# Optimization experiments

Measured on AMD Instinct MI355X. Metric: run time of the kernel, lower is better.

Reference implementation:

```python
import jax, jax.numpy as jnp
import numpy as np

N_HEADS = 16
N_KV_HEADS = 4
HEAD_DIM = 128  # d_model // n_heads = 2048 // 16
ROPE_THETA = 10000.0


def _rope_cos_sin(T, D, dtype):
    inv_freq = 1.0 / (ROPE_THETA ** (jnp.arange(0, D, 2, dtype=jnp.float32) / D))
    t = jnp.arange(T, dtype=jnp.float32)
    freqs = jnp.outer(t, inv_freq)               # [T, D/2]
    emb = jnp.concatenate([freqs, freqs], axis=-1)  # [T, D]
    return jnp.cos(emb).astype(dtype), jnp.sin(emb).astype(dtype)


def _rotate_half(x):
    x1, x2 = jnp.split(x, 2, axis=-1)
    return jnp.concatenate([-x2, x1], axis=-1)


def setup_inputs() -> dict:
    key = jax.random.key(0)
    k1, k2, k3, k4, k5 = jax.random.split(key, 5)
    B, T, C = 2, 2048, 2048
    H, KV, D = N_HEADS, N_KV_HEADS, HEAD_DIM
    s = 0.02
    return {
        "x": jax.random.normal(k1, (B, T, C), dtype=jnp.float32),
        "Wq": jax.random.normal(k2, (C, H * D), dtype=jnp.float32) * s,
        "Wk": jax.random.normal(k3, (C, KV * D), dtype=jnp.float32) * s,
        "Wv": jax.random.normal(k4, (C, KV * D), dtype=jnp.float32) * s,
        "Wo": jax.random.normal(k5, (H * D, C), dtype=jnp.float32) * s,
    }


def reference(x, Wq, Wk, Wv, Wo):
    B, T, C = x.shape
    H, KV, D = N_HEADS, N_KV_HEADS, HEAD_DIM
    G = H // KV
    scale = D ** -0.5

    q = (x @ Wq).reshape(B, T, H, D).transpose(0, 2, 1, 3)    # [B,H,T,D]
    k = (x @ Wk).reshape(B, T, KV, D).transpose(0, 2, 1, 3)   # [B,KV,T,D]
    v = (x @ Wv).reshape(B, T, KV, D).transpose(0, 2, 1, 3)   # [B,KV,T,D]

    cos, sin = _rope_cos_sin(T, D, x.dtype)  # [T,D] each, broadcasts over B,H
    q = q * cos + _rotate_half(q) * sin
    k = k * cos + _rotate_half(k) * sin

    # repeat_interleave kv heads to match query heads
    k = jnp.repeat(k, G, axis=1)  # [B,H,T,D]
    v = jnp.repeat(v, G, axis=1)  # [B,H,T,D]

    scores = jnp.einsum('bhqd,bhkd->bhqk', q, k) * scale  # [B,H,T,T]
    causal = jnp.tril(jnp.ones((T, T), dtype=bool))
    scores = jnp.where(causal, scores, jnp.finfo(scores.dtype).min)
    attn = jax.nn.softmax(scores, axis=-1)

    out = jnp.einsum('bhqk,bhkd->bhqd', attn, v)           # [B,H,T,D]
    out = out.transpose(0, 2, 1, 3).reshape(B, T, H * D)    # [B,T,C]
    return out @ Wo
```

## Files before the change

### kernel.cpp

```cpp
#include <hip/hip_runtime.h>
#include <cstdint>
#include <cstddef>

typedef __attribute__((ext_vector_type(4))) float f32x4;
typedef __attribute__((ext_vector_type(8))) short s16x8;
typedef __attribute__((ext_vector_type(4))) short s16x4;

#define B_  2
#define T_  2048
#define C_  2048
#define H_  16
#define KV_ 4
#define D_  128
#define M_  4096

static __device__ __forceinline__ float bf2f(ushort u){
  union { float f; uint32_t u; } x; x.u = ((uint32_t)u) << 16; return x.f;
}
static __device__ __forceinline__ ushort f2bf(float f){
  union { float f; uint32_t u; } x; x.f = f;
  uint32_t r = x.u + 0x7FFF + ((x.u >> 16) & 1);
  return (ushort)(r >> 16);
}

static __device__ __forceinline__ void gl_lds16(const ushort* g, ushort* s){
  __builtin_amdgcn_global_load_lds((const __attribute__((address_space(1))) void*)g,
                                   (__attribute__((address_space(3))) void*)s, 16, 0, 0);
}

__global__ void cvt_f32_bf16(const float* __restrict__ in, ushort* __restrict__ out, int n4){
  int idx = blockIdx.x * blockDim.x + threadIdx.x;
  int stride = gridDim.x * blockDim.x;
  for (int i = idx; i < n4; i += stride){
    float4 v = ((const float4*)in)[i];
    s16x4 o;
    o[0] = (short)f2bf(v.x); o[1] = (short)f2bf(v.y);
    o[2] = (short)f2bf(v.z); o[3] = (short)f2bf(v.w);
    ((s16x4*)out)[i] = o;
  }
}

__global__ void transpose_all(const float* __restrict__ Wq, const float* __restrict__ Wk,
                              const float* __restrict__ Wv, const float* __restrict__ Wo,
                              ushort* __restrict__ Wcat, ushort* __restrict__ Wot){
  __shared__ float tile[32][33];
  int bx = blockIdx.x;
  const float* W; ushort* Wt; int N; int n0;
  if (bx < 64)      { W = Wq; Wt = Wcat;                          N = 2048; n0 = bx * 32; }
  else if (bx < 80) { W = Wk; Wt = Wcat + (size_t)2048 * 2048;    N = 512;  n0 = (bx - 64) * 32; }
  else if (bx < 96) { W = Wv; Wt = Wcat + (size_t)2560 * 2048;    N = 512;  n0 = (bx - 80) * 32; }
  else              { W = Wo; Wt = Wot;                           N = 2048; n0 = (bx - 96) * 32; }
  int k0 = blockIdx.y * 32;
  int tx = threadIdx.x, ty = threadIdx.y;
  #pragma unroll
  for (int r = 0; r < 4; r++)
    tile[ty + 8*r][tx] = W[(size_t)(k0 + ty + 8*r) * N + n0 + tx];
  __syncthreads();
  #pragma unroll
  for (int r = 0; r < 4; r++)
    Wt[(size_t)(n0 + ty + 8*r) * 2048 + k0 + tx] = f2bf(tile[tx][ty + 8*r]);
}

template<int MODE>
__global__ __launch_bounds__(512)
void gemm_deep(const ushort* __restrict__ A, const ushort* __restrict__ Bt,
               void* __restrict__ C0, void* __restrict__ C1, void* __restrict__ C2,
               int N, int Kd, int nbx){
  __shared__ __align__(16) ushort Abuf[4][8192];
  __shared__ __align__(16) ushort Bbuf[4][8192];
  int tid = threadIdx.x, w = tid >> 6, l = tid & 63;
  int l15 = l & 15, l4 = l >> 4;

  int cpx = gridDim.x >> 3;
  int logical = (blockIdx.x & 7) * cpx + (blockIdx.x >> 3);
  int bx = logical % nbx, by = logical / nbx;
  int rblk = by * 128, cblk = bx * 128;
  int wm = w & 1, wn = w >> 1;

  int sr = tid >> 3;
  int sc = ((tid & 7) * 8) ^ ((sr & 7) << 3);
  const ushort* gA = A  + (size_t)(rblk + sr) * Kd + sc;
  const ushort* gB = Bt + (size_t)(cblk + sr) * Kd + sc;
  size_t rowK = (size_t)64 * Kd;
  int wb = w * 512;

  auto stage = [&](int t){
    int bsel = t & 3; int koff = t * 64;
    gl_lds16(gA + koff,        &Abuf[bsel][wb]);
    gl_lds16(gA + rowK + koff, &Abuf[bsel][4096 + wb]);
    gl_lds16(gB + koff,        &Bbuf[bsel][wb]);
    gl_lds16(gB + rowK + koff, &Bbuf[bsel][4096 + wb]);
  };

  int arow = wm * 64 + l15;
  int brow = wn * 32 + l15;
  int kx0 = (l4 * 8) ^ ((l15 & 7) << 3);
  int kx1 = (32 + l4 * 8) ^ ((l15 & 7) << 3);

  f32x4 acc[4][2] = {};

  auto phase = [&](int t, int dostage, int vm){
    const ushort* Ab = Abuf[t & 3];
    const ushort* Bb = Bbuf[t & 3];
    s16x8 a[4][2], b[2][2];
    #pragma unroll
    for (int m = 0; m < 4; m++){
      a[m][0] = *(const s16x8*)(Ab + (arow + m*16) * 64 + kx0);
      a[m][1] = *(const s16x8*)(Ab + (arow + m*16) * 64 + kx1);
    }
    #pragma unroll
    for (int n = 0; n < 2; n++){
      b[n][0] = *(const s16x8*)(Bb + (brow + n*16) * 64 + kx0);
      b[n][1] = *(const s16x8*)(Bb + (brow + n*16) * 64 + kx1);
    }
    if (dostage) stage(t + 3);
    if (vm == 8)      { asm volatile("s_waitcnt vmcnt(8)" ::: "memory"); }
    else if (vm == 4) { asm volatile("s_waitcnt vmcnt(4)" ::: "memory"); }
    else if (vm == 0) { asm volatile("s_waitcnt vmcnt(0)" ::: "memory"); }
    asm volatile("s_waitcnt lgkmcnt(0)" ::: "memory");
    __builtin_amdgcn_sched_barrier(0);
    __builtin_amdgcn_s_barrier();
    __builtin_amdgcn_s_setprio(1);
    #pragma unroll
    for (int m = 0; m < 4; m++)
      #pragma unroll
      for (int n = 0; n < 2; n++){
        acc[m][n] = __builtin_amdgcn_mfma_f32_16x16x32_bf16(a[m][0], b[n][0], acc[m][n], 0, 0, 0);
        acc[m][n] = __builtin_amdgcn_mfma_f32_16x16x32_bf16(a[m][1], b[n][1], acc[m][n], 0, 0, 0);
      }
    __builtin_amdgcn_s_setprio(0);
  };

  stage(0); stage(1); stage(2);
  asm volatile("s_waitcnt vmcnt(8)" ::: "memory");
  __builtin_amdgcn_s_barrier();

  int nt = Kd >> 6;
  #pragma unroll 1
  for (int t = 0; t < nt - 3; ++t) phase(t, 1, 8);
  phase(nt - 3, 0, 4);
  phase(nt - 2, 0, 0);
  phase(nt - 1, 0, -1);

  #pragma unroll
  for (int m = 0; m < 4; m++){
    #pragma unroll
    for (int n = 0; n < 2; n++){
      #pragma unroll
      for (int j = 0; j < 4; j++){
        int row = rblk + wm*64 + m*16 + l4*4 + j;
        int col = cblk + wn*32 + n*16 + l15;
        float v = acc[m][n][j];
        if (MODE == 0){
          ((float*)C0)[(size_t)row * N + col] = v;
        } else {
          int t = row & (T_ - 1), bb = row >> 11;
          ushort bv = f2bf(v);
          if (col < 2048){
            int hh = col >> 7, d = col & 127;
            ((ushort*)C0)[(((size_t)(bb * H_ + hh)) * T_ + t) * D_ + d] = bv;
          } else if (col < 2560){
            int c2 = col - 2048;
            int hh = c2 >> 7, d = c2 & 127;
            ((ushort*)C1)[(((size_t)(bb * KV_ + hh)) * T_ + t) * D_ + d] = bv;
          } else {
            int c2 = col - 2560;
            int hh = c2 >> 7, d = c2 & 127;
            ((ushort*)C2)[(((size_t)(bb * KV_ + hh)) * D_ + d) * T_ + t] = bv;
          }
        }
      }
    }
  }
}

__global__ __launch_bounds__(256)
void rope_all(ushort* __restrict__ Qb, ushort* __restrict__ Kb, float sq){
  int y = blockIdx.y;
  ushort* X; int bh; float scale;
  if (y < B_ * H_){ X = Qb; bh = y;           scale = sq;  }
  else            { X = Kb; bh = y - B_ * H_; scale = 1.f; }
  int tr = threadIdx.x >> 4;
  int j  = threadIdx.x & 15;
  int t  = blockIdx.x * 16 + tr;
  ushort* row = X + ((size_t)bh * T_ + t) * D_;
  s16x4 lo = *(const s16x4*)(row + j*4);
  s16x4 hi = *(const s16x4*)(row + 64 + j*4);
  s16x4 olo, ohi;
  #pragma unroll
  for (int i = 0; i < 4; i++){
    int d = j*4 + i;
    float invf = exp2f(-(float)d * 0.2076205059304602f);
    float s, c;
    __sincosf((float)t * invf, &s, &c);
    float q1 = bf2f((ushort)lo[i]);
    float q2 = bf2f((ushort)hi[i]);
    olo[i] = (short)f2bf((q1 * c - q2 * s) * scale);
    ohi[i] = (short)f2bf((q2 * c + q1 * s) * scale);
  }
  *(s16x4*)(row + j*4) = olo;
  *(s16x4*)(row + 64 + j*4) = ohi;
}

__global__ __launch_bounds__(512, 4)
void attn_kernel4(const ushort* __restrict__ Q, const ushort* __restrict__ Kc,
                  const ushort* __restrict__ Vt, ushort* __restrict__ O){
  __shared__ __align__(16) ushort Ks[64 * 128];
  __shared__ __align__(16) ushort Vs[128 * 64];
  __shared__ __align__(16) ushort Ps[8 * 16 * 64];
  int bid = blockIdx.x;
  int i  = bid >> 3;
  int qt = (i < 32) ? (63 - i) : (i - 32);
  int sub = bid & 7;
  int b = sub >> 2, kvh = sub & 3;
  int tid = threadIdx.x, w = tid >> 6, l = tid & 63;
  int l15 = l & 15, l4 = l >> 4;
  int sw3 = (l15 & 7) << 3;
  int q0 = qt * 32;
  int hq = kvh * 4 + (w >> 1);
  int qrow0 = q0 + (w & 1) * 16;
  int qrow = qrow0 + l15;

  s16x8 qf[4];
  const ushort* qbase = Q + (((size_t)(b * H_ + hq)) * T_ + qrow) * D_;
  #pragma unroll
  for (int kk = 0; kk < 4; kk++)
    qf[kk] = *(const s16x8*)(qbase + kk * 32 + l4 * 8);

  f32x4 oacc[8] = {};
  float mrun = -1e30f;
  float rsum = 0.f;
  const float THR = 11.5415603f;
  ushort* Pw = Ps + w * (16 * 64) + l15 * 64;

  const ushort* kbase = Kc + ((size_t)(b * KV_ + kvh)) * T_ * D_;
  const ushort* vbase = Vt + ((size_t)(b * KV_ + kvh)) * D_ * T_;
  int jmax = (q0 + 31) >> 6;

  int kr0 = tid >> 4, kcb = tid & 15;
  int vd0 = tid >> 3, vtb = tid & 7;
  int ksoff = kr0 * 128 + ((kcb * 8) ^ ((kr0 & 7) << 3));
  int vsoff = vd0 * 64  + ((vtb * 8) ^ ((vd0 & 7) << 3));
  const ushort* kg = kbase + (size_t)kr0 * D_ + kcb * 8;
  const ushort* vg = vbase + (size_t)vd0 * T_ + vtb * 8;

  s16x8 kreg0, kreg1, vreg0, vreg1;
  kreg0 = *(const s16x8*)(kg);
  kreg1 = *(const s16x8*)(kg + (size_t)32 * D_);
  vreg0 = *(const s16x8*)(vg);
  vreg1 = *(const s16x8*)(vg + (size_t)64 * T_);

  for (int jt = 0; jt <= jmax; jt++){
    __syncthreads();
    *(s16x8*)(Ks + ksoff)            = kreg0;
    *(s16x8*)(Ks + ksoff + 32 * 128) = kreg1;
    *(s16x8*)(Vs + vsoff)            = vreg0;
    *(s16x8*)(Vs + vsoff + 64 * 64)  = vreg1;
    __syncthreads();
    if (jt < jmax){
      int k1 = (jt + 1) * 64;
      kreg0 = *(const s16x8*)(kg + (size_t)k1 * D_);
      kreg1 = *(const s16x8*)(kg + (size_t)(k1 + 32) * D_);
      vreg0 = *(const s16x8*)(vg + k1);
      vreg1 = *(const s16x8*)(vg + (size_t)64 * T_ + k1);
    }
    int k0 = jt * 64;

    f32x4 sacc[4] = {};
    __builtin_amdgcn_s_setprio(1);
    #pragma unroll
    for (int kk = 0; kk < 4; kk++){
      #pragma unroll
      for (int n = 0; n < 4; n++){
        s16x8 kf = *(const s16x8*)(Ks + (16*n + l15) * 128 + ((kk*32 + l4*8) ^ sw3));
        sacc[n] = __builtin_amdgcn_mfma_f32_16x16x32_bf16(kf, qf[kk], sacc[n], 0, 0, 0);
      }
    }
    __builtin_amdgcn_s_setprio(0);
    if (jt == jmax){
      #pragma unroll
      for (int n = 0; n < 4; n++)
        #pragma unroll
        for (int j = 0; j < 4; j++){
          int kcol = k0 + 16*n + 4*l4 + j;
          if (kcol > qrow) sacc[n][j] = -1e30f;
        }
    }
    float mloc = -1e30f;
    #pragma unroll
    for (int n = 0; n < 4; n++)
      #pragma unroll
      for (int j = 0; j < 4; j++)
        mloc = fmaxf(mloc, sacc[n][j]);
    if (__any((int)(mloc > mrun + THR))){
      float m2 = fmaxf(mloc, __shfl_xor(mloc, 16));
      m2 = fmaxf(m2, __shfl_xor(m2, 32));
      float mnew = fmaxf(mrun, m2);
      float alpha = exp2f(mrun - mnew);
      mrun = mnew;
      rsum *= alpha;
      #pragma unroll
      for (int n8 = 0; n8 < 8; n8++)
        #pragma unroll
        for (int j = 0; j < 4; j++)
          oacc[n8][j] *= alpha;
    }
    #pragma unroll
    for (int n = 0; n < 4; n++){
      s16x4 pk;
      #pragma unroll
      for (int j = 0; j < 4; j++){
        float p = exp2f(sacc[n][j] - mrun);
        rsum += p;
        pk[j] = (short)f2bf(p);
      }
      *(s16x4*)(Pw + ((16*n + 4*l4) ^ sw3)) = pk;
    }
    __builtin_amdgcn_s_setprio(1);
    #pragma unroll
    for (int kk = 0; kk < 2; kk++){
      s16x8 pf = *(const s16x8*)(Pw + ((kk*32 + l4*8) ^ sw3));
      #pragma unroll
      for (int n8 = 0; n8 < 8; n8++){
        s16x8 vf = *(const s16x8*)(Vs + (16*n8 + l15) * 64 + ((kk*32 + l4*8) ^ sw3));
        oacc[n8] = __builtin_amdgcn_mfma_f32_16x16x32_bf16(vf, pf, oacc[n8], 0, 0, 0);
      }
    }
    __builtin_amdgcn_s_setprio(0);
  }

  rsum += __shfl_xor(rsum, 16);
  rsum += __shfl_xor(rsum, 32);
  float inv = 1.f / rsum;
  ushort* obase = O + ((size_t)(b * T_ + qrow)) * C_ + hq * D_ + 4*l4;
  #pragma unroll
  for (int n8 = 0; n8 < 8; n8++){
    s16x4 ov;
    #pragma unroll
    for (int j = 0; j < 4; j++)
      ov[j] = (short)f2bf(oacc[n8][j] * inv);
    *(s16x4*)(obase + 16*n8) = ov;
  }
}

extern "C" void kernel_launch(void* const* d_in, const int* in_sizes, int n_in,
                              void* d_out, int out_size, void* d_ws, size_t ws_size,
                              hipStream_t stream){
  const float* x  = (const float*)d_in[0];
  const float* Wq = (const float*)d_in[1];
  const float* Wk = (const float*)d_in[2];
  const float* Wv = (const float*)d_in[3];
  const float* Wo = (const float*)d_in[4];
  float* out = (float*)d_out;

  char* ws = (char*)d_ws;
  size_t off = 0;
  auto alloc = [&](size_t bytes)->void*{
    void* p = ws + off; off += (bytes + 255) & ~(size_t)255; return p;
  };
  ushort* xb   = (ushort*)alloc((size_t)M_ * C_ * 2);
  ushort* Wcat = (ushort*)alloc((size_t)3072 * 2048 * 2);
  ushort* Wot  = (ushort*)alloc((size_t)2048 * 2048 * 2);
  ushort* Qb   = (ushort*)alloc((size_t)B_ * H_ * T_ * D_ * 2);
  ushort* Kb   = (ushort*)alloc((size_t)B_ * KV_ * T_ * D_ * 2);
  ushort* Vtb  = (ushort*)alloc((size_t)B_ * KV_ * T_ * D_ * 2);
  ushort* Ob   = (ushort*)alloc((size_t)M_ * C_ * 2);

  cvt_f32_bf16<<<2048, 256, 0, stream>>>(x, xb, M_ * C_ / 4);
  transpose_all<<<dim3(160, 64), dim3(32, 8), 0, stream>>>(Wq, Wk, Wv, Wo, Wcat, Wot);

  gemm_deep<1><<<768, 512, 0, stream>>>(xb, Wcat, Qb, Kb, Vtb, 3072, 2048, 24);

  rope_all<<<dim3(T_/16, B_ * (H_ + KV_)), 256, 0, stream>>>(
      Qb, Kb, 0.08838834764831845f * 1.4426950408889634f);

  attn_kernel4<<<512, 512, 0, stream>>>(Qb, Kb, Vtb, Ob);

  gemm_deep<0><<<512, 512, 0, stream>>>(Ob, Wot, out, nullptr, nullptr, 2048, 2048, 16);
}
```

Measured before the change: 211.0 us.

## Process two query row groups per wave in attention with 256-thread blocks

The attention kernel now uses 4 waves per block, and each wave handles one query head over 32 query rows (two 16-row groups). Each K and V fragment read from shared memory then feeds two MFMAs, halving LDS fragment traffic per unit of compute. Softmax probabilities are packed to bf16 with a hardware v_cvt_pk_bf16_f32 instruction instead of manual rounding. The cost is roughly double the accumulator registers per wave and fewer waves per block to hide latency, with each thread loading four K/V chunks per tile instead of two.

```diff
diff --git a/kernel.cpp b/kernel.cpp
--- a/kernel.cpp
+++ b/kernel.cpp
@@ -202,12 +202,12 @@
   *(s16x4*)(row + 64 + j*4) = ohi;
 }
 
-__global__ __launch_bounds__(512, 4)
-void attn_kernel4(const ushort* __restrict__ Q, const ushort* __restrict__ Kc,
+__global__ __launch_bounds__(256)
+void attn_kernel5(const ushort* __restrict__ Q, const ushort* __restrict__ Kc,
                   const ushort* __restrict__ Vt, ushort* __restrict__ O){
   __shared__ __align__(16) ushort Ks[64 * 128];
   __shared__ __align__(16) ushort Vs[128 * 64];
-  __shared__ __align__(16) ushort Ps[8 * 16 * 64];
+  __shared__ __align__(16) ushort Ps[4 * 32 * 64];
   int bid = blockIdx.x;
   int i  = bid >> 3;
   int qt = (i < 32) ? (63 - i) : (i - 32);
@@ -217,21 +217,22 @@
   int l15 = l & 15, l4 = l >> 4;
   int sw3 = (l15 & 7) << 3;
   int q0 = qt * 32;
-  int hq = kvh * 4 + (w >> 1);
-  int qrow0 = q0 + (w & 1) * 16;
-  int qrow = qrow0 + l15;
-
-  s16x8 qf[4];
-  const ushort* qbase = Q + (((size_t)(b * H_ + hq)) * T_ + qrow) * D_;
-  #pragma unroll
-  for (int kk = 0; kk < 4; kk++)
-    qf[kk] = *(const s16x8*)(qbase + kk * 32 + l4 * 8);
-
-  f32x4 oacc[8] = {};
-  float mrun = -1e30f;
-  float rsum = 0.f;
+  int hq = kvh * 4 + w;
+
+  s16x8 qf[2][4];
+  #pragma unroll
+  for (int g = 0; g < 2; g++){
+    const ushort* qbase = Q + (((size_t)(b * H_ + hq)) * T_ + q0 + g*16 + l15) * D_;
+    #pragma unroll
+    for (int kk = 0; kk < 4; kk++)
+      qf[g][kk] = *(const s16x8*)(qbase + kk * 32 + l4 * 8);
+  }
+
+  f32x4 oacc[2][8] = {};
+  float mrun[2] = {-1e30f, -1e30f};
+  float rsum[2] = {0.f, 0.f};
   const float THR = 11.5415603f;
-  ushort* Pw = Ps + w * (16 * 64) + l15 * 64;
+  ushort* Pw = Ps + w * (32 * 64);
 
   const ushort* kbase = Kc + ((size_t)(b * KV_ + kvh)) * T_ * D_;
   const ushort* vbase = Vt + ((size_t)(b * KV_ + kvh)) * D_ * T_;
@@ -244,102 +245,131 @@
   const ushort* kg = kbase + (size_t)kr0 * D_ + kcb * 8;
   const ushort* vg = vbase + (size_t)vd0 * T_ + vtb * 8;
 
-  s16x8 kreg0, kreg1, vreg0, vreg1;
-  kreg0 = *(const s16x8*)(kg);
-  kreg1 = *(const s16x8*)(kg + (size_t)32 * D_);
-  vreg0 = *(const s16x8*)(vg);
-  vreg1 = *(const s16x8*)(vg + (size_t)64 * T_);
+  s16x8 kreg[4], vreg[4];
+  #pragma unroll
+  for (int c = 0; c < 4; c++){
+    kreg[c] = *(const s16x8*)(kg + (size_t)(c * 16) * D_);
+    vreg[c] = *(const s16x8*)(vg + (size_t)(c * 32) * T_);
+  }
 
   for (int jt = 0; jt <= jmax; jt++){
     __syncthreads();
-    *(s16x8*)(Ks + ksoff)            = kreg0;
-    *(s16x8*)(Ks + ksoff + 32 * 128) = kreg1;
-    *(s16x8*)(Vs + vsoff)            = vreg0;
-    *(s16x8*)(Vs + vsoff + 64 * 64)  = vreg1;
+    #pragma unroll
+    for (int c = 0; c < 4; c++){
+      *(s16x8*)(Ks + ksoff + c * 16 * 128) = kreg[c];
+      *(s16x8*)(Vs + vsoff + c * 32 * 64)  = vreg[c];
+    }
     __syncthreads();
     if (jt < jmax){
       int k1 = (jt + 1) * 64;
-      kreg0 = *(const s16x8*)(kg + (size_t)k1 * D_);
-      kreg1 = *(const s16x8*)(kg + (size_t)(k1 + 32) * D_);
-      vreg0 = *(const s16x8*)(vg + k1);
-      vreg1 = *(const s16x8*)(vg + (size_t)64 * T_ + k1);
+      #pragma unroll
+      for (int c = 0; c < 4; c++){
+        kreg[c] = *(const s16x8*)(kg + (size_t)(k1 + c * 16) * D_);
+        vreg[c] = *(const s16x8*)(vg + (size_t)(c * 32) * T_ + k1);
+      }
     }
     int k0 = jt * 64;
 
-    f32x4 sacc[4] = {};
+    f32x4 sacc[2][4] = {};
     __builtin_amdgcn_s_setprio(1);
     #pragma unroll
     for (int kk = 0; kk < 4; kk++){
       #pragma unroll
       for (int n = 0; n < 4; n++){
         s16x8 kf = *(const s16x8*)(Ks + (16*n + l15) * 128 + ((kk*32 + l4*8) ^ sw3));
-        sacc[n] = __builtin_amdgcn_mfma_f32_16x16x32_bf16(kf, qf[kk], sacc[n], 0, 0, 0);
+        sacc[0][n] = __builtin_amdgcn_mfma_f32_16x16x32_bf16(kf, qf[0][kk], sacc[0][n], 0, 0, 0);
+        sacc[1][n] = __builtin_amdgcn_mfma_f32_16x16x32_bf16(kf, qf[1][kk], sacc[1][n], 0, 0, 0);
       }
     }
     __builtin_amdgcn_s_setprio(0);
     if (jt == jmax){
       #pragma unroll
+      for (int g = 0; g < 2; g++){
+        int qrow = q0 + g*16 + l15;
+        #pragma unroll
+        for (int n = 0; n < 4; n++)
+          #pragma unroll
+          for (int j = 0; j < 4; j++){
+            int kcol = k0 + 16*n + 4*l4 + j;
+            if (kcol > qrow) sacc[g][n][j] = -1e30f;
+          }
+      }
+    }
+    float mloc[2];
+    #pragma unroll
+    for (int g = 0; g < 2; g++){
+      float m = -1e30f;
+      #pragma unroll
       for (int n = 0; n < 4; n++)
         #pragma unroll
-        for (int j = 0; j < 4; j++){
-          int kcol = k0 + 16*n + 4*l4 + j;
-          if (kcol > qrow) sacc[n][j] = -1e30f;
-        }
-    }
-    float mloc = -1e30f;
-    #pragma unroll
-    for (int n = 0; n < 4; n++)
-      #pragma unroll
-      for (int j = 0; j < 4; j++)
-        mloc = fmaxf(mloc, sacc[n][j]);
-    if (__any((int)(mloc > mrun + THR))){
-      float m2 = fmaxf(mloc, __shfl_xor(mloc, 16));
-      m2 = fmaxf(m2, __shfl_xor(m2, 32));
-      float mnew = fmaxf(mrun, m2);
-      float alpha = exp2f(mrun - mnew);
-      mrun = mnew;
-      rsum *= alpha;
-      #pragma unroll
-      for (int n8 = 0; n8 < 8; n8++)
+        for (int j = 0; j < 4; j++)
+          m = fmaxf(m, sacc[g][n][j]);
+      mloc[g] = m;
+    }
+    if (__any((int)((mloc[0] > mrun[0] + THR) || (mloc[1] > mrun[1] + THR)))){
+      #pragma unroll
+      for (int g = 0; g < 2; g++){
+        float m2 = fmaxf(mloc[g], __shfl_xor(mloc[g], 16));
+        m2 = fmaxf(m2, __shfl_xor(m2, 32));
+        float mnew = fmaxf(mrun[g], m2);
+        float alpha = exp2f(mrun[g] - mnew);
+        mrun[g] = mnew;
+        rsum[g] *= alpha;
         #pragma unroll
-        for (int j = 0; j < 4; j++)
-          oacc[n8][j] *= alpha;
-    }
-    #pragma unroll
-    for (int n = 0; n < 4; n++){
-      s16x4 pk;
-      #pragma unroll
-      for (int j = 0; j < 4; j++){
-        float p = exp2f(sacc[n][j] - mrun);
-        rsum += p;
-        pk[j] = (short)f2bf(p);
-      }
-      *(s16x4*)(Pw + ((16*n + 4*l4) ^ sw3)) = pk;
+        for (int n8 = 0; n8 < 8; n8++)
+          #pragma unroll
+          for (int j = 0; j < 4; j++)
+            oacc[g][n8][j] *= alpha;
+      }
+    }
+    #pragma unroll
+    for (int g = 0; g < 2; g++){
+      ushort* Pg = Pw + (l15 + 16*g) * 64;
+      #pragma unroll
+      for (int n = 0; n < 4; n++){
+        float p0 = exp2f(sacc[g][n][0] - mrun[g]);
+        float p1 = exp2f(sacc[g][n][1] - mrun[g]);
+        float p2 = exp2f(sacc[g][n][2] - mrun[g]);
+        float p3 = exp2f(sacc[g][n][3] - mrun[g]);
+        rsum[g] += (p0 + p1) + (p2 + p3);
+        uint32_t lo, hi;
+        asm volatile("v_cvt_pk_bf16_f32 %0, %1, %2" : "=v"(lo) : "v"(p0), "v"(p1));
+        asm volatile("v_cvt_pk_bf16_f32 %0, %1, %2" : "=v"(hi) : "v"(p2), "v"(p3));
+        uint2 pk; pk.x = lo; pk.y = hi;
+        *(uint2*)(Pg + ((16*n + 4*l4) ^ sw3)) = pk;
+      }
     }
     __builtin_amdgcn_s_setprio(1);
     #pragma unroll
     for (int kk = 0; kk < 2; kk++){
-      s16x8 pf = *(const s16x8*)(Pw + ((kk*32 + l4*8) ^ sw3));
+      s16x8 pfA = *(const s16x8*)(Pw + l15 * 64        + ((kk*32 + l4*8) ^ sw3));
+      s16x8 pfB = *(const s16x8*)(Pw + (l15 + 16) * 64 + ((kk*32 + l4*8) ^ sw3));
       #pragma unroll
       for (int n8 = 0; n8 < 8; n8++){
         s16x8 vf = *(const s16x8*)(Vs + (16*n8 + l15) * 64 + ((kk*32 + l4*8) ^ sw3));
-        oacc[n8] = __builtin_amdgcn_mfma_f32_16x16x32_bf16(vf, pf, oacc[n8], 0, 0, 0);
+        oacc[0][n8] = __builtin_amdgcn_mfma_f32_16x16x32_bf16(vf, pfA, oacc[0][n8], 0, 0, 0);
+        oacc[1][n8] = __builtin_amdgcn_mfma_f32_16x16x32_bf16(vf, pfB, oacc[1][n8], 0, 0, 0);
       }
     }
     __builtin_amdgcn_s_setprio(0);
   }
 
-  rsum += __shfl_xor(rsum, 16);
-  rsum += __shfl_xor(rsum, 32);
-  float inv = 1.f / rsum;
-  ushort* obase = O + ((size_t)(b * T_ + qrow)) * C_ + hq * D_ + 4*l4;
-  #pragma unroll
-  for (int n8 = 0; n8 < 8; n8++){
-    s16x4 ov;
-    #pragma unroll
-    for (int j = 0; j < 4; j++)
-      ov[j] = (short)f2bf(oacc[n8][j] * inv);
-    *(s16x4*)(obase + 16*n8) = ov;
+  #pragma unroll
+  for (int g = 0; g < 2; g++){
+    float r = rsum[g];
+    r += __shfl_xor(r, 16);
+    r += __shfl_xor(r, 32);
+    float inv = 1.f / r;
+    int qrow = q0 + g*16 + l15;
+    ushort* obase = O + ((size_t)(b * T_ + qrow)) * C_ + hq * D_ + 4*l4;
+    #pragma unroll
+    for (int n8 = 0; n8 < 8; n8++){
+      s16x4 ov;
+      #pragma unroll
+      for (int j = 0; j < 4; j++)
+        ov[j] = (short)f2bf(oacc[g][n8][j] * inv);
+      *(s16x4*)(obase + 16*n8) = ov;
+    }
   }
 }
 
@@ -374,7 +404,7 @@
   rope_all<<<dim3(T_/16, B_ * (H_ + KV_)), 256, 0, stream>>>(
       Qb, Kb, 0.08838834764831845f * 1.4426950408889634f);
 
-  attn_kernel4<<<512, 512, 0, stream>>>(Qb, Kb, Vtb, Ob);
+  attn_kernel5<<<512, 256, 0, stream>>>(Qb, Kb, Vtb, Ob);
 
   gemm_deep<0><<<512, 512, 0, stream>>>(Ob, Wot, out, nullptr, nullptr, 2048, 2048, 16);
 }
```

After: 239.7 us. 13.6% more time.

## Restructure GEMM to 256 threads with 64x64 warp tiles and 32-wide K stages

Applied to the files above, without the earlier changes.

The GEMM kernel drops from 8 to 4 waves per block. Each wave now computes a 64x64 output tile with a 4x4 MFMA accumulator grid, and K is staged in 32-element slices, which halves LDS use per block and changes the swizzle. This raises register reuse per wave and could allow more blocks per CU, at the cost of more accumulator registers and more pipeline iterations with barriers. Separately, the attention softmax now packs P to bf16 with the hardware v_cvt_pk_bf16_f32 instruction instead of manual rounding.

```diff
diff --git a/kernel.cpp b/kernel.cpp
--- a/kernel.cpp
+++ b/kernel.cpp
@@ -62,12 +62,12 @@
 }
 
 template<int MODE>
-__global__ __launch_bounds__(512)
-void gemm_deep(const ushort* __restrict__ A, const ushort* __restrict__ Bt,
-               void* __restrict__ C0, void* __restrict__ C1, void* __restrict__ C2,
-               int N, int Kd, int nbx){
-  __shared__ __align__(16) ushort Abuf[4][8192];
-  __shared__ __align__(16) ushort Bbuf[4][8192];
+__global__ __launch_bounds__(256)
+void gemm_ht(const ushort* __restrict__ A, const ushort* __restrict__ Bt,
+             void* __restrict__ C0, void* __restrict__ C1, void* __restrict__ C2,
+             int N, int Kd, int nbx){
+  __shared__ __align__(16) ushort Ab[4][4096];
+  __shared__ __align__(16) ushort Bb[4][4096];
   int tid = threadIdx.x, w = tid >> 6, l = tid & 63;
   int l15 = l & 15, l4 = l >> 4;
 
@@ -77,43 +77,39 @@
   int rblk = by * 128, cblk = bx * 128;
   int wm = w & 1, wn = w >> 1;
 
-  int sr = tid >> 3;
-  int sc = ((tid & 7) * 8) ^ ((sr & 7) << 3);
+  int sr = tid >> 2;
+  int sc = (((tid & 3) ^ ((sr >> 1) & 3)) * 8);
   const ushort* gA = A  + (size_t)(rblk + sr) * Kd + sc;
   const ushort* gB = Bt + (size_t)(cblk + sr) * Kd + sc;
   size_t rowK = (size_t)64 * Kd;
   int wb = w * 512;
 
-  auto stage = [&](int t){
-    int bsel = t & 3; int koff = t * 64;
-    gl_lds16(gA + koff,        &Abuf[bsel][wb]);
-    gl_lds16(gA + rowK + koff, &Abuf[bsel][4096 + wb]);
-    gl_lds16(gB + koff,        &Bbuf[bsel][wb]);
-    gl_lds16(gB + rowK + koff, &Bbuf[bsel][4096 + wb]);
+  auto stage = [&](int H){
+    int slot = H & 3;
+    int koff = H * 32;
+    gl_lds16(gA + koff,        &Ab[slot][wb]);
+    gl_lds16(gA + rowK + koff, &Ab[slot][2048 + wb]);
+    gl_lds16(gB + koff,        &Bb[slot][wb]);
+    gl_lds16(gB + rowK + koff, &Bb[slot][2048 + wb]);
   };
 
   int arow = wm * 64 + l15;
-  int brow = wn * 32 + l15;
-  int kx0 = (l4 * 8) ^ ((l15 & 7) << 3);
-  int kx1 = (32 + l4 * 8) ^ ((l15 & 7) << 3);
-
-  f32x4 acc[4][2] = {};
-
-  auto phase = [&](int t, int dostage, int vm){
-    const ushort* Ab = Abuf[t & 3];
-    const ushort* Bb = Bbuf[t & 3];
-    s16x8 a[4][2], b[2][2];
-    #pragma unroll
-    for (int m = 0; m < 4; m++){
-      a[m][0] = *(const s16x8*)(Ab + (arow + m*16) * 64 + kx0);
-      a[m][1] = *(const s16x8*)(Ab + (arow + m*16) * 64 + kx1);
-    }
-    #pragma unroll
-    for (int n = 0; n < 2; n++){
-      b[n][0] = *(const s16x8*)(Bb + (brow + n*16) * 64 + kx0);
-      b[n][1] = *(const s16x8*)(Bb + (brow + n*16) * 64 + kx1);
-    }
-    if (dostage) stage(t + 3);
+  int brow = wn * 64 + l15;
+  int kxs = (l4 ^ ((l15 >> 1) & 3)) * 8;
+
+  f32x4 acc[4][4] = {};
+
+  auto phase = [&](int H, int dostage, int vm){
+    const ushort* Ah = Ab[H & 3];
+    const ushort* Bh = Bb[H & 3];
+    s16x8 a[4], b[4];
+    #pragma unroll
+    for (int m = 0; m < 4; m++)
+      a[m] = *(const s16x8*)(Ah + (arow + m*16) * 32 + kxs);
+    #pragma unroll
+    for (int n = 0; n < 4; n++)
+      b[n] = *(const s16x8*)(Bh + (brow + n*16) * 32 + kxs);
+    if (dostage) stage(H + 3);
     if (vm == 8)      { asm volatile("s_waitcnt vmcnt(8)" ::: "memory"); }
     else if (vm == 4) { asm volatile("s_waitcnt vmcnt(4)" ::: "memory"); }
     else if (vm == 0) { asm volatile("s_waitcnt vmcnt(0)" ::: "memory"); }
@@ -124,10 +120,8 @@
     #pragma unroll
     for (int m = 0; m < 4; m++)
       #pragma unroll
-      for (int n = 0; n < 2; n++){
-        acc[m][n] = __builtin_amdgcn_mfma_f32_16x16x32_bf16(a[m][0], b[n][0], acc[m][n], 0, 0, 0);
-        acc[m][n] = __builtin_amdgcn_mfma_f32_16x16x32_bf16(a[m][1], b[n][1], acc[m][n], 0, 0, 0);
-      }
+      for (int n = 0; n < 4; n++)
+        acc[m][n] = __builtin_amdgcn_mfma_f32_16x16x32_bf16(a[m], b[n], acc[m][n], 0, 0, 0);
     __builtin_amdgcn_s_setprio(0);
   };
 
@@ -135,21 +129,21 @@
   asm volatile("s_waitcnt vmcnt(8)" ::: "memory");
   __builtin_amdgcn_s_barrier();
 
-  int nt = Kd >> 6;
+  int nH = Kd >> 5;
   #pragma unroll 1
-  for (int t = 0; t < nt - 3; ++t) phase(t, 1, 8);
-  phase(nt - 3, 0, 4);
-  phase(nt - 2, 0, 0);
-  phase(nt - 1, 0, -1);
+  for (int H = 0; H < nH - 3; ++H) phase(H, 1, 8);
+  phase(nH - 3, 0, 4);
+  phase(nH - 2, 0, 0);
+  phase(nH - 1, 0, -1);
 
   #pragma unroll
   for (int m = 0; m < 4; m++){
     #pragma unroll
-    for (int n = 0; n < 2; n++){
+    for (int n = 0; n < 4; n++){
       #pragma unroll
       for (int j = 0; j < 4; j++){
         int row = rblk + wm*64 + m*16 + l4*4 + j;
-        int col = cblk + wn*32 + n*16 + l15;
+        int col = cblk + wn*64 + n*16 + l15;
         float v = acc[m][n][j];
         if (MODE == 0){
           ((float*)C0)[(size_t)row * N + col] = v;
@@ -307,14 +301,16 @@
     }
     #pragma unroll
     for (int n = 0; n < 4; n++){
-      s16x4 pk;
-      #pragma unroll
-      for (int j = 0; j < 4; j++){
-        float p = exp2f(sacc[n][j] - mrun);
-        rsum += p;
-        pk[j] = (short)f2bf(p);
-      }
-      *(s16x4*)(Pw + ((16*n + 4*l4) ^ sw3)) = pk;
+      float p0 = exp2f(sacc[n][0] - mrun);
+      float p1 = exp2f(sacc[n][1] - mrun);
+      float p2 = exp2f(sacc[n][2] - mrun);
+      float p3 = exp2f(sacc[n][3] - mrun);
+      rsum += (p0 + p1) + (p2 + p3);
+      uint32_t lo, hi;
+      asm volatile("v_cvt_pk_bf16_f32 %0, %1, %2" : "=v"(lo) : "v"(p0), "v"(p1));
+      asm volatile("v_cvt_pk_bf16_f32 %0, %1, %2" : "=v"(hi) : "v"(p2), "v"(p3));
+      uint2 pk; pk.x = lo; pk.y = hi;
+      *(uint2*)(Pw + ((16*n + 4*l4) ^ sw3)) = pk;
     }
     __builtin_amdgcn_s_setprio(1);
     #pragma unroll
@@ -369,12 +365,12 @@
   cvt_f32_bf16<<<2048, 256, 0, stream>>>(x, xb, M_ * C_ / 4);
   transpose_all<<<dim3(160, 64), dim3(32, 8), 0, stream>>>(Wq, Wk, Wv, Wo, Wcat, Wot);
 
-  gemm_deep<1><<<768, 512, 0, stream>>>(xb, Wcat, Qb, Kb, Vtb, 3072, 2048, 24);
+  gemm_ht<1><<<768, 256, 0, stream>>>(xb, Wcat, Qb, Kb, Vtb, 3072, 2048, 24);
 
   rope_all<<<dim3(T_/16, B_ * (H_ + KV_)), 256, 0, stream>>>(
       Qb, Kb, 0.08838834764831845f * 1.4426950408889634f);
 
   attn_kernel4<<<512, 512, 0, stream>>>(Qb, Kb, Vtb, Ob);
 
-  gemm_deep<0><<<512, 512, 0, stream>>>(Ob, Wot, out, nullptr, nullptr, 2048, 2048, 16);
-}
+  gemm_ht<0><<<512, 256, 0, stream>>>(Ob, Wot, out, nullptr, nullptr, 2048, 2048, 16);
+}
```

New measurement: 215.2 us. 1.02x slower.

## Load V fragments directly from global into registers, skipping LDS staging

Applied to the files above, without the earlier changes.

The attention kernel no longer stages V tiles through shared memory. Each wave now loads its MFMA V fragments straight from global memory into registers at the start of every key tile. The softmax probabilities are also packed to bf16 with the hardware v_cvt_pk_bf16_f32 instruction instead of manual rounding. This removes the LDS writes and reads for V and frees shared memory. The cost is that each wave fetches V itself, so traffic is duplicated across the 8 waves, loads land on the critical path without prefetch, and register pressure rises.

```diff
diff --git a/kernel.cpp b/kernel.cpp
--- a/kernel.cpp
+++ b/kernel.cpp
@@ -203,10 +203,9 @@
 }
 
 __global__ __launch_bounds__(512, 4)
-void attn_kernel4(const ushort* __restrict__ Q, const ushort* __restrict__ Kc,
+void attn_kernel6(const ushort* __restrict__ Q, const ushort* __restrict__ Kc,
                   const ushort* __restrict__ Vt, ushort* __restrict__ O){
   __shared__ __align__(16) ushort Ks[64 * 128];
-  __shared__ __align__(16) ushort Vs[128 * 64];
   __shared__ __align__(16) ushort Ps[8 * 16 * 64];
   int bid = blockIdx.x;
   int i  = bid >> 3;
@@ -238,33 +237,32 @@
   int jmax = (q0 + 31) >> 6;
 
   int kr0 = tid >> 4, kcb = tid & 15;
-  int vd0 = tid >> 3, vtb = tid & 7;
   int ksoff = kr0 * 128 + ((kcb * 8) ^ ((kr0 & 7) << 3));
-  int vsoff = vd0 * 64  + ((vtb * 8) ^ ((vd0 & 7) << 3));
   const ushort* kg = kbase + (size_t)kr0 * D_ + kcb * 8;
-  const ushort* vg = vbase + (size_t)vd0 * T_ + vtb * 8;
-
-  s16x8 kreg0, kreg1, vreg0, vreg1;
+
+  const ushort* vfb = vbase + (size_t)l15 * T_ + l4 * 8;
+
+  s16x8 kreg0, kreg1;
   kreg0 = *(const s16x8*)(kg);
   kreg1 = *(const s16x8*)(kg + (size_t)32 * D_);
-  vreg0 = *(const s16x8*)(vg);
-  vreg1 = *(const s16x8*)(vg + (size_t)64 * T_);
 
   for (int jt = 0; jt <= jmax; jt++){
     __syncthreads();
     *(s16x8*)(Ks + ksoff)            = kreg0;
     *(s16x8*)(Ks + ksoff + 32 * 128) = kreg1;
-    *(s16x8*)(Vs + vsoff)            = vreg0;
-    *(s16x8*)(Vs + vsoff + 64 * 64)  = vreg1;
     __syncthreads();
+    int k0 = jt * 64;
+    s16x8 vfr0[8], vfr1[8];
+    #pragma unroll
+    for (int n8 = 0; n8 < 8; n8++){
+      vfr0[n8] = *(const s16x8*)(vfb + (size_t)(16*n8) * T_ + k0);
+      vfr1[n8] = *(const s16x8*)(vfb + (size_t)(16*n8) * T_ + k0 + 32);
+    }
     if (jt < jmax){
       int k1 = (jt + 1) * 64;
       kreg0 = *(const s16x8*)(kg + (size_t)k1 * D_);
       kreg1 = *(const s16x8*)(kg + (size_t)(k1 + 32) * D_);
-      vreg0 = *(const s16x8*)(vg + k1);
-      vreg1 = *(const s16x8*)(vg + (size_t)64 * T_ + k1);
-    }
-    int k0 = jt * 64;
+    }
 
     f32x4 sacc[4] = {};
     __builtin_amdgcn_s_setprio(1);
@@ -307,24 +305,27 @@
     }
     #pragma unroll
     for (int n = 0; n < 4; n++){
-      s16x4 pk;
-      #pragma unroll
-      for (int j = 0; j < 4; j++){
-        float p = exp2f(sacc[n][j] - mrun);
-        rsum += p;
-        pk[j] = (short)f2bf(p);
-      }
-      *(s16x4*)(Pw + ((16*n + 4*l4) ^ sw3)) = pk;
+      float p0 = exp2f(sacc[n][0] - mrun);
+      float p1 = exp2f(sacc[n][1] - mrun);
+      float p2 = exp2f(sacc[n][2] - mrun);
+      float p3 = exp2f(sacc[n][3] - mrun);
+      rsum += (p0 + p1) + (p2 + p3);
+      uint32_t lo, hi;
+      asm volatile("v_cvt_pk_bf16_f32 %0, %1, %2" : "=v"(lo) : "v"(p0), "v"(p1));
+      asm volatile("v_cvt_pk_bf16_f32 %0, %1, %2" : "=v"(hi) : "v"(p2), "v"(p3));
+      uint2 pk; pk.x = lo; pk.y = hi;
+      *(uint2*)(Pw + ((16*n + 4*l4) ^ sw3)) = pk;
     }
     __builtin_amdgcn_s_setprio(1);
-    #pragma unroll
-    for (int kk = 0; kk < 2; kk++){
-      s16x8 pf = *(const s16x8*)(Pw + ((kk*32 + l4*8) ^ sw3));
-      #pragma unroll
-      for (int n8 = 0; n8 < 8; n8++){
-        s16x8 vf = *(const s16x8*)(Vs + (16*n8 + l15) * 64 + ((kk*32 + l4*8) ^ sw3));
-        oacc[n8] = __builtin_amdgcn_mfma_f32_16x16x32_bf16(vf, pf, oacc[n8], 0, 0, 0);
-      }
+    {
+      s16x8 pf0 = *(const s16x8*)(Pw + ((l4*8) ^ sw3));
+      s16x8 pf1 = *(const s16x8*)(Pw + ((32 + l4*8) ^ sw3));
+      #pragma unroll
+      for (int n8 = 0; n8 < 8; n8++)
+        oacc[n8] = __builtin_amdgcn_mfma_f32_16x16x32_bf16(vfr0[n8], pf0, oacc[n8], 0, 0, 0);
+      #pragma unroll
+      for (int n8 = 0; n8 < 8; n8++)
+        oacc[n8] = __builtin_amdgcn_mfma_f32_16x16x32_bf16(vfr1[n8], pf1, oacc[n8], 0, 0, 0);
     }
     __builtin_amdgcn_s_setprio(0);
   }
@@ -374,7 +375,7 @@
   rope_all<<<dim3(T_/16, B_ * (H_ + KV_)), 256, 0, stream>>>(
       Qb, Kb, 0.08838834764831845f * 1.4426950408889634f);
 
-  attn_kernel4<<<512, 512, 0, stream>>>(Qb, Kb, Vtb, Ob);
+  attn_kernel6<<<512, 512, 0, stream>>>(Qb, Kb, Vtb, Ob);
 
   gemm_deep<0><<<512, 512, 0, stream>>>(Ob, Wot, out, nullptr, nullptr, 2048, 2048, 16);
 }
```

After: 415.0 us. 96.7% more time.
